# Optimization experiments

Measured on AMD Instinct MI355X. Metric: run time of the kernel, lower is better.

## Reference

```python
import jax, jax.numpy as jnp
import numpy as np

B = 32; H = 56; W = 56; C = 384; NH = 12; WS = 7; SS = 3
N = WS * WS            # tokens per window = 49
NW = (H // WS) * (W // WS)  # windows per image = 64
HD = C // NH           # head dim = 32
MLP_H = 4 * C
EPS = 1e-5


def _rel_pos_index():
    coords = np.stack(np.meshgrid(np.arange(WS), np.arange(WS), indexing='ij'))
    cf = coords.reshape(2, -1)                      # (2, N)
    rel = cf[:, :, None] - cf[:, None, :]           # (2, N, N)
    rel = rel.transpose(1, 2, 0).astype(np.int64)   # (N, N, 2)
    rel[..., 0] += WS - 1
    rel[..., 1] += WS - 1
    rel[..., 0] *= 2 * WS - 1
    return rel.sum(-1)                               # (N, N)


def _attn_mask():
    img = np.zeros((H, W))
    cnt = 0
    slc = (slice(0, -WS), slice(-WS, -SS), slice(-SS, None))
    for hs in slc:
        for ws in slc:
            img[hs, ws] = cnt
            cnt += 1
    mw = img.reshape(H // WS, WS, W // WS, WS).transpose(0, 2, 1, 3).reshape(-1, N)  # (NW, N)
    diff = mw[:, None, :] - mw[:, :, None]
    return np.where(diff != 0, -100.0, 0.0).astype(np.float32)  # (NW, N, N)


_RPI = jnp.asarray(_rel_pos_index())
_MASK = jnp.asarray(_attn_mask())


def _ln(x, w, b):
    m = jnp.mean(x, axis=-1, keepdims=True)
    v = jnp.mean((x - m) ** 2, axis=-1, keepdims=True)
    return (x - m) * jax.lax.rsqrt(v + EPS) * w + b


def _window_partition(x):  # (B,H,W,C) -> (B*NW, WS, WS, C)
    x = x.reshape(B, H // WS, WS, W // WS, WS, C)
    return x.transpose(0, 1, 3, 2, 4, 5).reshape(-1, WS, WS, C)


def _window_reverse(xw):  # (B*NW, WS, WS, C) -> (B,H,W,C)
    x = xw.reshape(B, H // WS, W // WS, WS, WS, C)
    return x.transpose(0, 1, 3, 2, 4, 5).reshape(B, H, W, C)


def setup_inputs() -> dict:
    key = jax.random.key(0)
    ks = jax.random.split(key, 8)
    s = 0.02
    return {
        'x': jax.random.normal(ks[0], (B, H * W, C), jnp.float32),
        'norm1_w': jnp.ones((C,), jnp.float32),
        'norm1_b': jnp.zeros((C,), jnp.float32),
        'qkv_w': jax.random.normal(ks[1], (C, 3 * C), jnp.float32) * s,
        'qkv_b': jnp.zeros((3 * C,), jnp.float32),
        'rpb_table': jax.random.normal(ks[2], ((2 * WS - 1) * (2 * WS - 1), NH), jnp.float32) * s,
        'proj_w': jax.random.normal(ks[3], (C, C), jnp.float32) * s,
        'proj_b': jnp.zeros((C,), jnp.float32),
        'norm2_w': jnp.ones((C,), jnp.float32),
        'norm2_b': jnp.zeros((C,), jnp.float32),
        'fc1_w': jax.random.normal(ks[4], (C, MLP_H), jnp.float32) * s,
        'fc1_b': jnp.zeros((MLP_H,), jnp.float32),
        'fc2_w': jax.random.normal(ks[5], (MLP_H, C), jnp.float32) * s,
        'fc2_b': jnp.zeros((C,), jnp.float32),
    }


def reference(x, norm1_w, norm1_b, qkv_w, qkv_b, rpb_table, proj_w, proj_b,
              norm2_w, norm2_b, fc1_w, fc1_b, fc2_w, fc2_b):
    shortcut = x
    xn = _ln(x, norm1_w, norm1_b).reshape(B, H, W, C)
    # cyclic shift
    xs = jnp.roll(xn, shift=(-SS, -SS), axis=(1, 2))
    xw = _window_partition(xs).reshape(-1, N, C)           # (B*NW, N, C)

    qkv = (xw @ qkv_w + qkv_b).reshape(-1, N, 3, NH, HD)
    qkv = qkv.transpose(2, 0, 3, 1, 4)                      # (3, B*NW, NH, N, HD)
    q, k, v = qkv[0], qkv[1], qkv[2]
    q = q * (HD ** -0.5)
    attn = jnp.einsum('bhnd,bhmd->bhnm', q, k)              # (B*NW, NH, N, N)

    bias = rpb_table[_RPI.reshape(-1)].reshape(N, N, NH).transpose(2, 0, 1)
    attn = attn + bias[None]
    # shift mask: (NW, N, N) broadcast over batch and heads
    attn = attn.reshape(B, NW, NH, N, N) + _MASK[None, :, None]
    attn = jax.nn.softmax(attn.reshape(-1, NH, N, N), axis=-1)

    out = jnp.einsum('bhnm,bhmd->bhnd', attn, v)            # (B*NW, NH, N, HD)
    out = out.transpose(0, 2, 1, 3).reshape(-1, N, C)
    out = out @ proj_w + proj_b

    out = _window_reverse(out.reshape(-1, WS, WS, C))
    out = jnp.roll(out, shift=(SS, SS), axis=(1, 2)).reshape(B, H * W, C)

    x = shortcut + out
    h = _ln(x, norm2_w, norm2_b)
    h = jax.nn.gelu(h @ fc1_w + fc1_b, approximate=False) @ fc2_w + fc2_b
    return x + h
```

## Files before the change

kernel.cpp:

```cpp
#include <hip/hip_runtime.h>
#include <hip/hip_bf16.h>
#include <math.h>


typedef short bf16x8 __attribute__((ext_vector_type(8)));
typedef float f32x4 __attribute__((ext_vector_type(4)));

#define GLOAD_LDS16(g, s)                                                      \
    __builtin_amdgcn_global_load_lds(                                          \
        (const __attribute__((address_space(1))) void*)(g),                    \
        (__attribute__((address_space(3))) void*)(s), 16, 0, 0)

__global__ __launch_bounds__(256) void prep_k(
    const float* __restrict__ qkvw, const float* __restrict__ projw,
    const float* __restrict__ fc1w, const float* __restrict__ fc2w,
    const float* __restrict__ rpb,
    __hip_bfloat16* __restrict__ wt_qkv, __hip_bfloat16* __restrict__ wt_proj,
    __hip_bfloat16* __restrict__ wt_fc1, __hip_bfloat16* __restrict__ wt_fc2,
    float* __restrict__ biasM) {
    int id = blockIdx.x * 256 + threadIdx.x;
    if (id < 442368) {
        int k = id / 1152, n = id % 1152;
        wt_qkv[(size_t)n * 384 + k] = __float2bfloat16(qkvw[id]);
        return;
    }
    id -= 442368;
    if (id < 147456) {
        int k = id / 384, n = id % 384;
        wt_proj[(size_t)n * 384 + k] = __float2bfloat16(projw[id]);
        return;
    }
    id -= 147456;
    if (id < 589824) {
        int k = id / 1536, n = id % 1536;
        wt_fc1[(size_t)n * 384 + k] = __float2bfloat16(fc1w[id]);
        return;
    }
    id -= 589824;
    if (id < 589824) {
        int k = id / 384, n = id % 384;
        wt_fc2[(size_t)n * 1536 + k] = __float2bfloat16(fc2w[id]);
        return;
    }
    id -= 589824;
    if (id < 28812) {
        int h = id / 2401, rem = id % 2401, i = rem / 49, j = rem % 49;
        int ih = i / 7, iw = i % 7, jh = j / 7, jw = j % 7;
        int idx = (ih - jh + 6) * 13 + (iw - jw + 6);
        biasM[id] = rpb[idx * 12 + h];
    }
}

template <int MODE>
__global__ __launch_bounds__(256) void ln_k(const float* __restrict__ X,
                                            const float* __restrict__ w,
                                            const float* __restrict__ b,
                                            __hip_bfloat16* __restrict__ out) {
    int wv = threadIdx.x >> 6, lane = threadIdx.x & 63;
    int row = blockIdx.x * 4 + wv;
    size_t src_row;
    if (MODE == 0) {
        int wi = row / 49, t = row % 49;
        int bb = wi >> 6, wrem = wi & 63;
        int wh = wrem >> 3, ww = wrem & 7;
        int th = t / 7, tw = t % 7;
        int hi = (wh * 7 + th + 3) % 56;
        int wimg = (ww * 7 + tw + 3) % 56;
        src_row = (size_t)(bb * 3136 + hi * 56 + wimg);
    } else {
        src_row = row;
    }
    const float* src = X + src_row * 384;
    float v[6];
    float s = 0.f, sq = 0.f;
#pragma unroll
    for (int i = 0; i < 6; i++) {
        v[i] = src[lane + i * 64];
        s += v[i];
        sq += v[i] * v[i];
    }
#pragma unroll
    for (int m = 32; m >= 1; m >>= 1) {
        s += __shfl_xor(s, m, 64);
        sq += __shfl_xor(sq, m, 64);
    }
    float mean = s * (1.f / 384.f);
    float var = sq * (1.f / 384.f) - mean * mean;
    float rstd = rsqrtf(var + 1e-5f);
    size_t orow = (size_t)row * 384;
#pragma unroll
    for (int i = 0; i < 6; i++) {
        int c = lane + i * 64;
        out[orow + c] = __float2bfloat16((v[i] - mean) * rstd * w[c] + b[c]);
    }
}

template <int EPI>
__global__ __launch_bounds__(256) void gemm_k(
    const __hip_bfloat16* __restrict__ A, const __hip_bfloat16* __restrict__ Bt,
    const float* __restrict__ bias, int K, int nTilesN,
    __hip_bfloat16* outb, float* outf, const float* resin) {
    __shared__ __align__(16) __hip_bfloat16 Asm[3][128 * 32];
    __shared__ __align__(16) __hip_bfloat16 Bsm[3][128 * 32];
    int bid = blockIdx.x;
    bid = (bid & 7) * ((int)gridDim.x >> 3) + (bid >> 3);
    int tM = bid / nTilesN, tN = bid % nTilesN;
    size_t m0 = (size_t)tM * 128;
    int n0 = tN * 128;
    int tid = threadIdx.x, wv = tid >> 6, lane = tid & 63;
    int wr = wv >> 1, wc = wv & 1;
    int lm = lane & 15, lg = lane >> 4;

    f32x4 acc[4][4];
#pragma unroll
    for (int i = 0; i < 4; i++)
#pragma unroll
        for (int j = 0; j < 4; j++) acc[i][j] = (f32x4){0.f, 0.f, 0.f, 0.f};

    int c0 = wv * 2;
    int rA0 = c0 * 16 + (lane >> 2);
    int kk = (((lane & 3) ^ ((lane >> 3) & 3)) * 8);
    const __hip_bfloat16* Ap = A + (m0 + rA0) * K + kk;
    const __hip_bfloat16* Bp = Bt + (size_t)(n0 + rA0) * K + kk;
    int lgs8 = (lg ^ ((lm >> 1) & 3)) * 8;

    int nkt = K >> 5;
#define STAGE(buf, kt_)                                                        \
    {                                                                          \
        int k0_ = (kt_) << 5;                                                  \
        GLOAD_LDS16(Ap + k0_, &Asm[buf][c0 * 512]);                            \
        GLOAD_LDS16(Ap + (size_t)16 * K + k0_, &Asm[buf][(c0 + 1) * 512]);     \
        GLOAD_LDS16(Bp + k0_, &Bsm[buf][c0 * 512]);                            \
        GLOAD_LDS16(Bp + (size_t)16 * K + k0_, &Bsm[buf][(c0 + 1) * 512]);     \
    }
    STAGE(0, 0)
    STAGE(1, 1)
    int cur = 0;
    for (int kt = 0; kt < nkt; kt++) {
        if (kt + 1 < nkt) {
            asm volatile("s_waitcnt vmcnt(4)" ::: "memory");
        } else {
            asm volatile("s_waitcnt vmcnt(0)" ::: "memory");
        }
        __builtin_amdgcn_s_barrier();
        asm volatile("" ::: "memory");
        if (kt + 2 < nkt) {
            int b2 = cur + 2;
            if (b2 >= 3) b2 -= 3;
            STAGE(b2, kt + 2)
        }
        bf16x8 af[4], bfg[4];
#pragma unroll
        for (int i = 0; i < 4; i++)
            af[i] = *(const bf16x8*)&Asm[cur][(wr * 64 + i * 16 + lm) * 32 + lgs8];
#pragma unroll
        for (int j = 0; j < 4; j++)
            bfg[j] = *(const bf16x8*)&Bsm[cur][(wc * 64 + j * 16 + lm) * 32 + lgs8];
#pragma unroll
        for (int i = 0; i < 4; i++)
#pragma unroll
            for (int j = 0; j < 4; j++)
                acc[i][j] = __builtin_amdgcn_mfma_f32_16x16x32_bf16(
                    af[i], bfg[j], acc[i][j], 0, 0, 0);
        cur++;
        if (cur == 3) cur = 0;
    }
#undef STAGE

    int ld = nTilesN * 128;
#pragma unroll
    for (int i = 0; i < 4; i++) {
#pragma unroll
        for (int r = 0; r < 4; r++) {
            int row = (int)m0 + wr * 64 + i * 16 + lg * 4 + r;
#pragma unroll
            for (int j = 0; j < 4; j++) {
                int col = n0 + wc * 64 + j * 16 + lm;
                float val = acc[i][j][r] + bias[col];
                if (EPI == 0) {
                    outb[(size_t)row * ld + col] = __float2bfloat16(val);
                } else if (EPI == 2) {
                    float g = 0.5f * val * (1.f + erff(val * 0.70710678118f));
                    outb[(size_t)row * ld + col] = __float2bfloat16(g);
                } else if (EPI == 1) {
                    int wi = row / 49, t = row % 49;
                    int bb = wi >> 6, wrem = wi & 63;
                    int wh = wrem >> 3, ww = wrem & 7;
                    int th = t / 7, tw = t % 7;
                    int hi = (wh * 7 + th + 3) % 56;
                    int wimg = (ww * 7 + tw + 3) % 56;
                    size_t pos = (size_t)(bb * 3136 + hi * 56 + wimg) * 384 + col;
                    outf[pos] = resin[pos] + val;
                } else {
                    size_t pos = (size_t)row * 384 + col;
                    outf[pos] = resin[pos] + val;
                }
            }
        }
    }
}

__global__ __launch_bounds__(256) void attn_k(const __hip_bfloat16* __restrict__ qkv,
                                              const float* __restrict__ biasM,
                                              __hip_bfloat16* __restrict__ out) {
    __shared__ __align__(16) __hip_bfloat16 vt[32 * 72];
    __shared__ __align__(16) __hip_bfloat16 P[64 * 72];
    int bid = blockIdx.x;
    bid = (bid & 7) * ((int)gridDim.x >> 3) + (bid >> 3);
    int wi = bid / 12, h = bid % 12;
    int tid = threadIdx.x, wv = tid >> 6, lane = tid & 63;
    int lm = lane & 15, lg = lane >> 4;
    int wrem = wi & 63, wh = wrem >> 3, ww = wrem & 7;

#pragma unroll
    for (int i = 0; i < 9; i++) vt[tid * 9 + i] = __float2bfloat16(0.f);
    __syncthreads();
    if (tid < 196) {
        int t = tid >> 2, d0 = (tid & 3) * 8;
        bf16x8 vv = *(const bf16x8*)(qkv + (size_t)(wi * 49 + t) * 1152 + 768 + h * 32 + d0);
#pragma unroll
        for (int i = 0; i < 8; i++) vt[(d0 + i) * 72 + t] = ((__hip_bfloat16*)&vv)[i];
    }

    int qrow = wv * 16 + lm;
    if (qrow > 48) qrow = 48;
    bf16x8 aq = *(const bf16x8*)(qkv + (size_t)(wi * 49 + qrow) * 1152 + h * 32 + lg * 8);
    f32x4 S[4];
#pragma unroll
    for (int ct = 0; ct < 4; ct++) {
        int krow = ct * 16 + lm;
        if (krow > 48) krow = 48;
        bf16x8 bk = *(const bf16x8*)(qkv + (size_t)(wi * 49 + krow) * 1152 + 384 + h * 32 + lg * 8);
        S[ct] = __builtin_amdgcn_mfma_f32_16x16x32_bf16(aq, bk, (f32x4){0.f, 0.f, 0.f, 0.f}, 0, 0, 0);
    }

    const float scale = 0.17677669529663687f;
#pragma unroll
    for (int r = 0; r < 4; r++) {
        int irow = wv * 16 + lg * 4 + r;
        int ic = irow <= 48 ? irow : 48;
        int ith = ic / 7, itw = ic % 7;
        int ihs = wh * 7 + ith, iws = ww * 7 + itw;
        int ridi = (ihs < 49 ? 0 : (ihs < 53 ? 1 : 2)) * 3 + (iws < 49 ? 0 : (iws < 53 ? 1 : 2));
        float vals[4];
        float mx = -1e30f;
#pragma unroll
        for (int ct = 0; ct < 4; ct++) {
            int jcol = ct * 16 + lm;
            float sv;
            if (jcol < 49) {
                int jth = jcol / 7, jtw = jcol % 7;
                int jhs = wh * 7 + jth, jws = ww * 7 + jtw;
                int ridj = (jhs < 49 ? 0 : (jhs < 53 ? 1 : 2)) * 3 + (jws < 49 ? 0 : (jws < 53 ? 1 : 2));
                sv = S[ct][r] * scale + biasM[h * 2401 + ic * 49 + jcol] +
                     (ridi != ridj ? -100.f : 0.f);
            } else {
                sv = -1e30f;
            }
            vals[ct] = sv;
            mx = fmaxf(mx, sv);
        }
#pragma unroll
        for (int m = 8; m >= 1; m >>= 1) mx = fmaxf(mx, __shfl_xor(mx, m, 64));
        float sum = 0.f;
#pragma unroll
        for (int ct = 0; ct < 4; ct++) {
            vals[ct] = __expf(vals[ct] - mx);
            sum += vals[ct];
        }
#pragma unroll
        for (int m = 8; m >= 1; m >>= 1) sum += __shfl_xor(sum, m, 64);
        float inv = 1.f / sum;
#pragma unroll
        for (int ct = 0; ct < 4; ct++)
            P[irow * 72 + ct * 16 + lm] = __float2bfloat16(vals[ct] * inv);
    }
    __syncthreads();

    f32x4 O[2] = {{0.f, 0.f, 0.f, 0.f}, {0.f, 0.f, 0.f, 0.f}};
#pragma unroll
    for (int ks = 0; ks < 2; ks++) {
        bf16x8 ap = *(const bf16x8*)&P[(wv * 16 + lm) * 72 + ks * 32 + lg * 8];
#pragma unroll
        for (int nt = 0; nt < 2; nt++) {
            bf16x8 bv = *(const bf16x8*)&vt[(nt * 16 + lm) * 72 + ks * 32 + lg * 8];
            O[nt] = __builtin_amdgcn_mfma_f32_16x16x32_bf16(ap, bv, O[nt], 0, 0, 0);
        }
    }
#pragma unroll
    for (int r = 0; r < 4; r++) {
        int row = wv * 16 + lg * 4 + r;
        if (row < 49) {
            size_t base = (size_t)(wi * 49 + row) * 384 + h * 32;
            out[base + lm] = __float2bfloat16(O[0][r]);
            out[base + 16 + lm] = __float2bfloat16(O[1][r]);
        }
    }
}

extern "C" void kernel_launch(void* const* d_in, const int* in_sizes, int n_in,
                              void* d_out, int out_size, void* d_ws, size_t ws_size,
                              hipStream_t stream) {
    (void)in_sizes; (void)n_in; (void)out_size; (void)ws_size;
    const float* x     = (const float*)d_in[0];
    const float* n1w   = (const float*)d_in[1];
    const float* n1b   = (const float*)d_in[2];
    const float* qkvw  = (const float*)d_in[3];
    const float* qkvb  = (const float*)d_in[4];
    const float* rpb   = (const float*)d_in[5];
    const float* projw = (const float*)d_in[6];
    const float* projb = (const float*)d_in[7];
    const float* n2w   = (const float*)d_in[8];
    const float* n2b   = (const float*)d_in[9];
    const float* fc1w  = (const float*)d_in[10];
    const float* fc1b  = (const float*)d_in[11];
    const float* fc2w  = (const float*)d_in[12];
    const float* fc2b  = (const float*)d_in[13];
    float* out = (float*)d_out;

    char* ws = (char*)d_ws;
    __hip_bfloat16* wt_qkv  = (__hip_bfloat16*)(ws + 0);
    __hip_bfloat16* wt_proj = (__hip_bfloat16*)(ws + 884736);
    __hip_bfloat16* wt_fc1  = (__hip_bfloat16*)(ws + 1179648);
    __hip_bfloat16* wt_fc2  = (__hip_bfloat16*)(ws + 2359296);
    float*          biasM   = (float*)(ws + 3538944);
    __hip_bfloat16* xw      = (__hip_bfloat16*)(ws + 3654656);
    __hip_bfloat16* qkv     = (__hip_bfloat16*)(ws + 80724992);
    __hip_bfloat16* attn_o  = (__hip_bfloat16*)(ws + 311936000);
    __hip_bfloat16* hidden  = xw;
    __hip_bfloat16* hn      = attn_o;

    prep_k<<<7025, 256, 0, stream>>>(qkvw, projw, fc1w, fc2w, rpb,
                                     wt_qkv, wt_proj, wt_fc1, wt_fc2, biasM);

    ln_k<0><<<25088, 256, 0, stream>>>(x, n1w, n1b, xw);
    gemm_k<0><<<784 * 9, 256, 0, stream>>>(xw, wt_qkv, qkvb, 384, 9, qkv, nullptr, nullptr);
    attn_k<<<2048 * 12, 256, 0, stream>>>(qkv, biasM, attn_o);
    gemm_k<1><<<784 * 3, 256, 0, stream>>>(attn_o, wt_proj, projb, 384, 3, nullptr, out, x);
    ln_k<1><<<25088, 256, 0, stream>>>(out, n2w, n2b, hn);
    gemm_k<2><<<784 * 12, 256, 0, stream>>>(hn, wt_fc1, fc1b, 384, 12, hidden, nullptr, nullptr);
    gemm_k<3><<<784 * 3, 256, 0, stream>>>(hidden, wt_fc2, fc2b, 1536, 3, nullptr, out, out);
}
```

Measured before the change: 1.306 ms.

## Restructure GEMM to 256x128 tiles with 8 waves and ping-pong LDS pipeline

The GEMM kernel moves from 128x128 tiles with 4 waves to 256x128 tiles with 8 waves and a K-step of 64. A and B get separate triple and double LDS buffers, the loop is unrolled six ways with explicit barriers, and s_setprio wraps the MFMA clusters so memory and math phases of different waves can interleave. The goal is better B-operand reuse and more latency hiding. In exchange it uses much more LDS, allows one block per CU, and adds more barriers. The K loop also assumes the number of K tiles is a multiple of 6, which holds for K=384 and K=1536.

```diff
diff --git a/kernel.cpp b/kernel.cpp
--- a/kernel.cpp
+++ b/kernel.cpp
@@ -10,6 +10,12 @@
     __builtin_amdgcn_global_load_lds(                                          \
         (const __attribute__((address_space(1))) void*)(g),                    \
         (__attribute__((address_space(3))) void*)(s), 16, 0, 0)
+
+#define SBAR()                                                                 \
+    {                                                                          \
+        __builtin_amdgcn_s_barrier();                                          \
+        __builtin_amdgcn_sched_barrier(0);                                     \
+    }
 
 __global__ __launch_bounds__(256) void prep_k(
     const float* __restrict__ qkvw, const float* __restrict__ projw,
@@ -96,16 +102,16 @@
 }
 
 template <int EPI>
-__global__ __launch_bounds__(256) void gemm_k(
+__global__ __launch_bounds__(512, 1) void gemm_k(
     const __hip_bfloat16* __restrict__ A, const __hip_bfloat16* __restrict__ Bt,
     const float* __restrict__ bias, int K, int nTilesN,
     __hip_bfloat16* outb, float* outf, const float* resin) {
-    __shared__ __align__(16) __hip_bfloat16 Asm[3][128 * 32];
-    __shared__ __align__(16) __hip_bfloat16 Bsm[3][128 * 32];
+    __shared__ __align__(16) __hip_bfloat16 Asm[3][256 * 64];
+    __shared__ __align__(16) __hip_bfloat16 Bsm[2][128 * 64];
     int bid = blockIdx.x;
     bid = (bid & 7) * ((int)gridDim.x >> 3) + (bid >> 3);
     int tM = bid / nTilesN, tN = bid % nTilesN;
-    size_t m0 = (size_t)tM * 128;
+    size_t m0 = (size_t)tM * 256;
     int n0 = tN * 128;
     int tid = threadIdx.x, wv = tid >> 6, lane = tid & 63;
     int wr = wv >> 1, wc = wv & 1;
@@ -117,55 +123,99 @@
 #pragma unroll
         for (int j = 0; j < 4; j++) acc[i][j] = (f32x4){0.f, 0.f, 0.f, 0.f};
 
-    int c0 = wv * 2;
-    int rA0 = c0 * 16 + (lane >> 2);
-    int kk = (((lane & 3) ^ ((lane >> 3) & 3)) * 8);
-    const __hip_bfloat16* Ap = A + (m0 + rA0) * K + kk;
-    const __hip_bfloat16* Bp = Bt + (size_t)(n0 + rA0) * K + kk;
-    int lgs8 = (lg ^ ((lm >> 1) & 3)) * 8;
-
-    int nkt = K >> 5;
-#define STAGE(buf, kt_)                                                        \
-    {                                                                          \
-        int k0_ = (kt_) << 5;                                                  \
-        GLOAD_LDS16(Ap + k0_, &Asm[buf][c0 * 512]);                            \
-        GLOAD_LDS16(Ap + (size_t)16 * K + k0_, &Asm[buf][(c0 + 1) * 512]);     \
-        GLOAD_LDS16(Bp + k0_, &Bsm[buf][c0 * 512]);                            \
-        GLOAD_LDS16(Bp + (size_t)16 * K + k0_, &Bsm[buf][(c0 + 1) * 512]);     \
-    }
-    STAGE(0, 0)
-    STAGE(1, 1)
-    int cur = 0;
-    for (int kt = 0; kt < nkt; kt++) {
-        if (kt + 1 < nkt) {
-            asm volatile("s_waitcnt vmcnt(4)" ::: "memory");
-        } else {
-            asm volatile("s_waitcnt vmcnt(0)" ::: "memory");
-        }
-        __builtin_amdgcn_s_barrier();
-        asm volatile("" ::: "memory");
-        if (kt + 2 < nkt) {
-            int b2 = cur + 2;
-            if (b2 >= 3) b2 -= 3;
-            STAGE(b2, kt + 2)
-        }
-        bf16x8 af[4], bfg[4];
-#pragma unroll
-        for (int i = 0; i < 4; i++)
-            af[i] = *(const bf16x8*)&Asm[cur][(wr * 64 + i * 16 + lm) * 32 + lgs8];
-#pragma unroll
-        for (int j = 0; j < 4; j++)
-            bfg[j] = *(const bf16x8*)&Bsm[cur][(wc * 64 + j * 16 + lm) * 32 + lgs8];
-#pragma unroll
-        for (int i = 0; i < 4; i++)
-#pragma unroll
-            for (int j = 0; j < 4; j++)
-                acc[i][j] = __builtin_amdgcn_mfma_f32_16x16x32_bf16(
-                    af[i], bfg[j], acc[i][j], 0, 0, 0);
-        cur++;
-        if (cur == 3) cur = 0;
-    }
-#undef STAGE
+    int srow = lane >> 3;
+    int sswz = ((lane & 7) ^ srow) * 8;
+    const __hip_bfloat16* pA = A + (m0 + wv * 32 + srow) * K + sswz;
+    const __hip_bfloat16* pB = Bt + (size_t)(n0 + wv * 16 + srow) * K + sswz;
+
+    int swz0 = ((0 + lg) ^ (lm & 7)) * 8;
+    int swz1 = ((4 + lg) ^ (lm & 7)) * 8;
+    int arow = (wr * 64 + lm) * 64;
+    int brow = (wc * 64 + lm) * 64;
+
+    int nkt = K >> 6;
+
+#define STAGE_A(buf, c, k2) \
+    GLOAD_LDS16(pA + (size_t)(c) * 8 * K + (k2), &Asm[buf][(wv * 4 + (c)) * 512])
+#define STAGE_B(buf, c, k2) \
+    GLOAD_LDS16(pB + (size_t)(c) * 8 * K + (k2), &Bsm[buf][(wv * 2 + (c)) * 512])
+
+    STAGE_B(0, 0, 0); STAGE_B(0, 1, 0);
+    STAGE_A(0, 0, 0); STAGE_A(0, 1, 0); STAGE_A(0, 2, 0); STAGE_A(0, 3, 0);
+    STAGE_A(1, 0, 64); STAGE_A(1, 1, 64); STAGE_A(1, 2, 64); STAGE_A(1, 3, 64);
+    asm volatile("s_waitcnt vmcnt(4)" ::: "memory");
+    SBAR();
+
+#define KTILE(CA, CB, T)                                                        \
+    {                                                                           \
+        constexpr int NA = ((CA) + 2) % 3;                                      \
+        constexpr int NB = (CB) ^ 1;                                            \
+        const __hip_bfloat16* aB = &Asm[CA][0];                                 \
+        const __hip_bfloat16* bB = &Bsm[CB][0];                                 \
+        const bool sta = (T) + 2 < nkt;                                         \
+        const bool stb = (T) + 1 < nkt;                                         \
+        const int k1 = ((T) + 1) << 6, k2 = ((T) + 2) << 6;                     \
+        bf16x8 vbf[4][2], vaA[2], vaB_[2], vaC[2], vaD[2];                      \
+        _Pragma("unroll") for (int j = 0; j < 4; j++) {                         \
+            vbf[j][0] = *(const bf16x8*)&bB[brow + j * 1024 + swz0];            \
+            vbf[j][1] = *(const bf16x8*)&bB[brow + j * 1024 + swz1];            \
+        }                                                                       \
+        vaA[0] = *(const bf16x8*)&aB[arow + swz0];                              \
+        vaA[1] = *(const bf16x8*)&aB[arow + swz1];                              \
+        vaB_[0] = *(const bf16x8*)&aB[arow + 1024 + swz0];                      \
+        vaB_[1] = *(const bf16x8*)&aB[arow + 1024 + swz1];                      \
+        if (stb) { STAGE_B(NB, 0, k1); STAGE_B(NB, 1, k1); }                    \
+        if (sta) {                                                              \
+            STAGE_A(NA, 0, k2); STAGE_A(NA, 1, k2);                             \
+            STAGE_A(NA, 2, k2); STAGE_A(NA, 3, k2);                             \
+        }                                                                       \
+        SBAR();                                                                 \
+        asm volatile("s_waitcnt lgkmcnt(0)" ::: "memory");                      \
+        __builtin_amdgcn_sched_barrier(0);                                      \
+        __builtin_amdgcn_s_setprio(1);                                          \
+        _Pragma("unroll") for (int kh = 0; kh < 2; kh++)                        \
+            _Pragma("unroll") for (int j = 0; j < 4; j++) {                     \
+                acc[0][j] = __builtin_amdgcn_mfma_f32_16x16x32_bf16(            \
+                    vaA[kh], vbf[j][kh], acc[0][j], 0, 0, 0);                   \
+                acc[1][j] = __builtin_amdgcn_mfma_f32_16x16x32_bf16(            \
+                    vaB_[kh], vbf[j][kh], acc[1][j], 0, 0, 0);                  \
+            }                                                                   \
+        __builtin_amdgcn_s_setprio(0);                                          \
+        SBAR();                                                                 \
+        vaC[0] = *(const bf16x8*)&aB[arow + 2048 + swz0];                       \
+        vaC[1] = *(const bf16x8*)&aB[arow + 2048 + swz1];                       \
+        vaD[0] = *(const bf16x8*)&aB[arow + 3072 + swz0];                       \
+        vaD[1] = *(const bf16x8*)&aB[arow + 3072 + swz1];                       \
+        SBAR();                                                                 \
+        asm volatile("s_waitcnt lgkmcnt(0)" ::: "memory");                      \
+        __builtin_amdgcn_sched_barrier(0);                                      \
+        __builtin_amdgcn_s_setprio(1);                                          \
+        _Pragma("unroll") for (int kh = 0; kh < 2; kh++)                        \
+            _Pragma("unroll") for (int j = 0; j < 4; j++) {                     \
+                acc[2][j] = __builtin_amdgcn_mfma_f32_16x16x32_bf16(            \
+                    vaC[kh], vbf[j][kh], acc[2][j], 0, 0, 0);                   \
+                acc[3][j] = __builtin_amdgcn_mfma_f32_16x16x32_bf16(            \
+                    vaD[kh], vbf[j][kh], acc[3][j], 0, 0, 0);                   \
+            }                                                                   \
+        __builtin_amdgcn_s_setprio(0);                                          \
+        if (stb) {                                                              \
+            if (sta) asm volatile("s_waitcnt vmcnt(4)" ::: "memory");           \
+            else     asm volatile("s_waitcnt vmcnt(0)" ::: "memory");           \
+            SBAR();                                                             \
+        }                                                                       \
+    }
+
+    for (int kt = 0; kt < nkt; kt += 6) {
+        KTILE(0, 0, kt)
+        KTILE(1, 1, kt + 1)
+        KTILE(2, 0, kt + 2)
+        KTILE(0, 1, kt + 3)
+        KTILE(1, 0, kt + 4)
+        KTILE(2, 1, kt + 5)
+    }
+#undef KTILE
+#undef STAGE_A
+#undef STAGE_B
 
     int ld = nTilesN * 128;
 #pragma unroll
@@ -334,10 +384,10 @@
                                      wt_qkv, wt_proj, wt_fc1, wt_fc2, biasM);
 
     ln_k<0><<<25088, 256, 0, stream>>>(x, n1w, n1b, xw);
-    gemm_k<0><<<784 * 9, 256, 0, stream>>>(xw, wt_qkv, qkvb, 384, 9, qkv, nullptr, nullptr);
+    gemm_k<0><<<392 * 9, 512, 0, stream>>>(xw, wt_qkv, qkvb, 384, 9, qkv, nullptr, nullptr);
     attn_k<<<2048 * 12, 256, 0, stream>>>(qkv, biasM, attn_o);
-    gemm_k<1><<<784 * 3, 256, 0, stream>>>(attn_o, wt_proj, projb, 384, 3, nullptr, out, x);
+    gemm_k<1><<<392 * 3, 512, 0, stream>>>(attn_o, wt_proj, projb, 384, 3, nullptr, out, x);
     ln_k<1><<<25088, 256, 0, stream>>>(out, n2w, n2b, hn);
-    gemm_k<2><<<784 * 12, 256, 0, stream>>>(hn, wt_fc1, fc1b, 384, 12, hidden, nullptr, nullptr);
-    gemm_k<3><<<784 * 3, 256, 0, stream>>>(hidden, wt_fc2, fc2b, 1536, 3, nullptr, out, out);
-}
+    gemm_k<2><<<392 * 12, 512, 0, stream>>>(hn, wt_fc1, fc1b, 384, 12, hidden, nullptr, nullptr);
+    gemm_k<3><<<392 * 3, 512, 0, stream>>>(hidden, wt_fc2, fc2b, 1536, 3, nullptr, out, out);
+}
```

New measurement: 1.337 ms. 1.02x slower.

## Restructure GEMM: register-held A fragments, LDS-only B, BK=64 double buffering

Applied to the files above, without the earlier changes.

The GEMM main loop is rewritten so each wave owns 32 full rows of the 128x128 tile and loads its A fragments straight from global memory into registers. Only the B operand is staged through LDS, with an XOR swizzle, a K-step of 64 and two buffers instead of three. Each B fragment read from LDS is now reused across two M sub-tiles, and launch bounds request two blocks per CU. In exchange, A is read directly from global without LDS sharing, there is higher register pressure, and B is staged through registers instead of async global-to-LDS loads.

```diff
diff --git a/kernel.cpp b/kernel.cpp
--- a/kernel.cpp
+++ b/kernel.cpp
@@ -5,11 +5,6 @@
 
 typedef short bf16x8 __attribute__((ext_vector_type(8)));
 typedef float f32x4 __attribute__((ext_vector_type(4)));
-
-#define GLOAD_LDS16(g, s)                                                      \
-    __builtin_amdgcn_global_load_lds(                                          \
-        (const __attribute__((address_space(1))) void*)(g),                    \
-        (__attribute__((address_space(3))) void*)(s), 16, 0, 0)
 
 __global__ __launch_bounds__(256) void prep_k(
     const float* __restrict__ qkvw, const float* __restrict__ projw,
@@ -96,87 +91,122 @@
 }
 
 template <int EPI>
-__global__ __launch_bounds__(256) void gemm_k(
+__global__ __launch_bounds__(256, 2) void gemm_k(
     const __hip_bfloat16* __restrict__ A, const __hip_bfloat16* __restrict__ Bt,
     const float* __restrict__ bias, int K, int nTilesN,
     __hip_bfloat16* outb, float* outf, const float* resin) {
-    __shared__ __align__(16) __hip_bfloat16 Asm[3][128 * 32];
-    __shared__ __align__(16) __hip_bfloat16 Bsm[3][128 * 32];
+    __shared__ __align__(16) __hip_bfloat16 lb[2][128 * 64];
     int bid = blockIdx.x;
     bid = (bid & 7) * ((int)gridDim.x >> 3) + (bid >> 3);
     int tM = bid / nTilesN, tN = bid % nTilesN;
     size_t m0 = (size_t)tM * 128;
     int n0 = tN * 128;
     int tid = threadIdx.x, wv = tid >> 6, lane = tid & 63;
-    int wr = wv >> 1, wc = wv & 1;
     int lm = lane & 15, lg = lane >> 4;
 
-    f32x4 acc[4][4];
+    f32x4 acc[2][8];
+#pragma unroll
+    for (int m = 0; m < 2; m++)
+#pragma unroll
+        for (int j = 0; j < 8; j++) acc[m][j] = (f32x4){0.f, 0.f, 0.f, 0.f};
+
+    const __hip_bfloat16* pA = A + (m0 + wv * 32 + lm) * K + lg * 8;
+    int brow = tid >> 1;
+    const __hip_bfloat16* pB = Bt + (size_t)(n0 + brow) * K + (tid & 1) * 32;
+    int wof[4];
 #pragma unroll
     for (int i = 0; i < 4; i++)
-#pragma unroll
-        for (int j = 0; j < 4; j++) acc[i][j] = (f32x4){0.f, 0.f, 0.f, 0.f};
-
-    int c0 = wv * 2;
-    int rA0 = c0 * 16 + (lane >> 2);
-    int kk = (((lane & 3) ^ ((lane >> 3) & 3)) * 8);
-    const __hip_bfloat16* Ap = A + (m0 + rA0) * K + kk;
-    const __hip_bfloat16* Bp = Bt + (size_t)(n0 + rA0) * K + kk;
-    int lgs8 = (lg ^ ((lm >> 1) & 3)) * 8;
-
-    int nkt = K >> 5;
-#define STAGE(buf, kt_)                                                        \
-    {                                                                          \
-        int k0_ = (kt_) << 5;                                                  \
-        GLOAD_LDS16(Ap + k0_, &Asm[buf][c0 * 512]);                            \
-        GLOAD_LDS16(Ap + (size_t)16 * K + k0_, &Asm[buf][(c0 + 1) * 512]);     \
-        GLOAD_LDS16(Bp + k0_, &Bsm[buf][c0 * 512]);                            \
-        GLOAD_LDS16(Bp + (size_t)16 * K + k0_, &Bsm[buf][(c0 + 1) * 512]);     \
-    }
-    STAGE(0, 0)
-    STAGE(1, 1)
-    int cur = 0;
-    for (int kt = 0; kt < nkt; kt++) {
-        if (kt + 1 < nkt) {
-            asm volatile("s_waitcnt vmcnt(4)" ::: "memory");
-        } else {
-            asm volatile("s_waitcnt vmcnt(0)" ::: "memory");
-        }
-        __builtin_amdgcn_s_barrier();
-        asm volatile("" ::: "memory");
-        if (kt + 2 < nkt) {
-            int b2 = cur + 2;
-            if (b2 >= 3) b2 -= 3;
-            STAGE(b2, kt + 2)
-        }
-        bf16x8 af[4], bfg[4];
-#pragma unroll
-        for (int i = 0; i < 4; i++)
-            af[i] = *(const bf16x8*)&Asm[cur][(wr * 64 + i * 16 + lm) * 32 + lgs8];
-#pragma unroll
-        for (int j = 0; j < 4; j++)
-            bfg[j] = *(const bf16x8*)&Bsm[cur][(wc * 64 + j * 16 + lm) * 32 + lgs8];
-#pragma unroll
-        for (int i = 0; i < 4; i++)
-#pragma unroll
-            for (int j = 0; j < 4; j++)
-                acc[i][j] = __builtin_amdgcn_mfma_f32_16x16x32_bf16(
-                    af[i], bfg[j], acc[i][j], 0, 0, 0);
-        cur++;
-        if (cur == 3) cur = 0;
-    }
-#undef STAGE
+        wof[i] = brow * 64 + ((((tid & 1) * 4 + i) ^ (brow & 7)) * 8);
+    int rof0 = ((0 + lg) ^ (lm & 7)) * 8;
+    int rof1 = ((4 + lg) ^ (lm & 7)) * 8;
+
+    int nkt = K >> 6;
+
+    bf16x8 bst[4];
+    bf16x8 aA[2][2], aB[2][2];
+
+#define LOADB(T)                                                               \
+    do {                                                                       \
+        const __hip_bfloat16* p_ = pB + (size_t)(T) * 64;                      \
+        bst[0] = *(const bf16x8*)(p_);                                         \
+        bst[1] = *(const bf16x8*)(p_ + 8);                                     \
+        bst[2] = *(const bf16x8*)(p_ + 16);                                    \
+        bst[3] = *(const bf16x8*)(p_ + 24);                                    \
+    } while (0)
+#define LOADA(DST, T)                                                          \
+    do {                                                                       \
+        const __hip_bfloat16* p_ = pA + (size_t)(T) * 64;                      \
+        DST[0][0] = *(const bf16x8*)(p_);                                      \
+        DST[0][1] = *(const bf16x8*)(p_ + 32);                                 \
+        DST[1][0] = *(const bf16x8*)(p_ + (size_t)16 * K);                     \
+        DST[1][1] = *(const bf16x8*)(p_ + (size_t)16 * K + 32);                \
+    } while (0)
+#define WRITEB(P)                                                              \
+    do {                                                                       \
+        *(bf16x8*)&lb[P][wof[0]] = bst[0];                                     \
+        *(bf16x8*)&lb[P][wof[1]] = bst[1];                                     \
+        *(bf16x8*)&lb[P][wof[2]] = bst[2];                                     \
+        *(bf16x8*)&lb[P][wof[3]] = bst[3];                                     \
+    } while (0)
+#define COMPUTE(P, AC)                                                         \
+    do {                                                                       \
+        _Pragma("unroll") for (int j = 0; j < 8; j++) {                        \
+            bf16x8 b0 = *(const bf16x8*)&lb[P][(j * 16 + lm) * 64 + rof0];     \
+            bf16x8 b1 = *(const bf16x8*)&lb[P][(j * 16 + lm) * 64 + rof1];     \
+            acc[0][j] = __builtin_amdgcn_mfma_f32_16x16x32_bf16(               \
+                AC[0][0], b0, acc[0][j], 0, 0, 0);                             \
+            acc[0][j] = __builtin_amdgcn_mfma_f32_16x16x32_bf16(               \
+                AC[0][1], b1, acc[0][j], 0, 0, 0);                             \
+            acc[1][j] = __builtin_amdgcn_mfma_f32_16x16x32_bf16(               \
+                AC[1][0], b0, acc[1][j], 0, 0, 0);                             \
+            acc[1][j] = __builtin_amdgcn_mfma_f32_16x16x32_bf16(               \
+                AC[1][1], b1, acc[1][j], 0, 0, 0);                             \
+        }                                                                      \
+    } while (0)
+#define ENDBAR()                                                               \
+    do {                                                                       \
+        asm volatile("s_waitcnt lgkmcnt(0)" ::: "memory");                     \
+        __builtin_amdgcn_sched_barrier(0);                                     \
+        __builtin_amdgcn_s_barrier();                                          \
+        __builtin_amdgcn_sched_barrier(0);                                     \
+    } while (0)
+#define ITER(P, AC, T)                                                         \
+    do {                                                                       \
+        if ((T) + 1 < nkt) WRITEB(P ^ 1);                                      \
+        if ((T) + 2 < nkt) LOADB((T) + 2);                                     \
+        COMPUTE(P, AC);                                                        \
+        if ((T) + 2 < nkt) LOADA(AC, (T) + 2);                                 \
+        ENDBAR();                                                              \
+    } while (0)
+
+    LOADB(0);
+    LOADA(aA, 0);
+    WRITEB(0);
+    LOADB(1);
+    LOADA(aB, 1);
+    ENDBAR();
+
+    for (int t = 0; t < nkt; t += 2) {
+        ITER(0, aA, t);
+        ITER(1, aB, t + 1);
+    }
+#undef ITER
+#undef ENDBAR
+#undef COMPUTE
+#undef WRITEB
+#undef LOADA
+#undef LOADB
 
     int ld = nTilesN * 128;
 #pragma unroll
-    for (int i = 0; i < 4; i++) {
+    for (int m = 0; m < 2; m++) {
 #pragma unroll
         for (int r = 0; r < 4; r++) {
-            int row = (int)m0 + wr * 64 + i * 16 + lg * 4 + r;
-#pragma unroll
-            for (int j = 0; j < 4; j++) {
-                int col = n0 + wc * 64 + j * 16 + lm;
-                float val = acc[i][j][r] + bias[col];
+            int row = (int)m0 + wv * 32 + m * 16 + lg * 4 + r;
+#pragma unroll
+            for (int j = 0; j < 8; j++) {
+                int col = n0 + j * 16 + lm;
+                float val = acc[m][j][r] + bias[col];
                 if (EPI == 0) {
                     outb[(size_t)row * ld + col] = __float2bfloat16(val);
                 } else if (EPI == 2) {
```

After: 1.309 ms. No clear change (+0.2%).
